# Kernel optimization log

Measured on AMD Instinct MI355X. Metric: run time of the kernel, lower is better.

Reference implementation:

```python
import jax, jax.numpy as jnp
import numpy as np

N, E, F, R, S = 20000, 320000, 64, 8, 10
AVG_NEIGH = 16.0


def setup_inputs() -> dict:
    key = jax.random.key(0)
    ks = jax.random.split(key, 16)
    inp = {
        "vectors": jax.random.normal(ks[0], (E, 3), jnp.float32),
        "node_feats": jax.random.normal(ks[1], (N, F, 4), jnp.float32),  # [N, F, 1(0e)+3(1o)]
        "node_specie": jax.random.randint(ks[2], (N,), 0, S),
        "radial_embedding": jax.random.normal(ks[3], (E, R), jnp.float32),
        "senders": jax.random.randint(ks[4], (E,), 0, N),
        "receivers": jax.random.randint(ks[5], (E,), 0, N),
        # residual FullyConnectedTensorProduct(feats, one-hot species 0e) == species-dep. linear per l
        "W_res_s": jax.random.normal(ks[6], (S, F, F), jnp.float32),
        "W_res_v": jax.random.normal(ks[7], (S, F, F), jnp.float32),
        # interaction block: input linear per l
        "W_in_s": jax.random.normal(ks[8], (F, F), jnp.float32),
        "W_in_v": jax.random.normal(ks[9], (F, F), jnp.float32),
        # radial MLP -> 5 CG tensor-product path weights per channel
        "mlp_w1": jax.random.normal(ks[10], (R, 64), jnp.float32),
        "mlp_w2": jax.random.normal(ks[11], (64, 5 * F), jnp.float32) / 8.0,
        # interaction block: output linear per l
        "W_out_s": jax.random.normal(ks[12], (F, F), jnp.float32),
        "W_out_v": jax.random.normal(ks[13], (F, F), jnp.float32),
        # symmetric product basis (correlation 3), species-dependent term weights
        "W_prod_s": jax.random.normal(ks[14], (S, 5, F), jnp.float32) * 0.3,
        "W_prod_v": jax.random.normal(ks[15], (S, 4, F), jnp.float32) * 0.3,
    }
    k2 = jax.random.split(jax.random.key(1), 3)
    inp["W_lin_s"] = jax.random.normal(k2[0], (F, F), jnp.float32)
    inp["W_lin_v"] = jax.random.normal(k2[1], (F, F), jnp.float32)
    inp["W_read"] = jax.random.normal(k2[2], (F, 1), jnp.float32)
    return inp


def _forward(vectors, node_feats, node_specie, radial_embedding, senders, receivers,
             W_res_s, W_res_v, W_in_s, W_in_v, mlp_w1, mlp_w2, W_out_s, W_out_v,
             W_prod_s, W_prod_v, W_lin_s, W_lin_v, W_read):
    inv_sf = 1.0 / jnp.sqrt(jnp.float32(F))
    s = node_feats[..., 0]          # [N,F]   0e channels
    v = node_feats[..., 1:]         # [N,F,3] 1o channels

    # --- residual connection: FCTP(feats, one-hot species 0e attrs) -> species-gated linear per l
    res_s = jnp.einsum('nf,ngf->ng', s, W_res_s[node_specie]) * inv_sf
    res_v = jnp.einsum('nfc,ngf->ngc', v, W_res_v[node_specie]) * inv_sf

    # --- InteractionBlock ---
    h_s = (s @ W_in_s) * inv_sf
    h_v = jnp.einsum('nfc,fg->ngc', v, W_in_v) * inv_sf

    # spherical harmonics up to max_ell=1: Y0 = 1, Y1 = unit edge vector
    r = jnp.sqrt(jnp.sum(vectors * vectors, -1) + 1e-12)
    Y1 = vectors / r[:, None]                                # [E,3]

    # radial MLP produces per-edge weights for the 5 CG paths:
    # (0e x Y0 -> 0e), (1o . Y1 -> 0e), (0e x Y1 -> 1o), (1o x Y0 -> 1o), (1o x Y1 -> 1o, cross)
    w = (jax.nn.silu(radial_embedding @ mlp_w1) @ mlp_w2).reshape(-1, 5, F)  # [E,5,F]

    ss = h_s[senders]                                        # [E,F]
    sv = h_v[senders]                                        # [E,F,3]
    dot = jnp.einsum('efc,ec->ef', sv, Y1)                   # [E,F]
    m_s = w[:, 0] * ss + w[:, 1] * dot                       # [E,F]
    m_v = (w[:, 2] * ss)[:, :, None] * Y1[:, None, :] \
        + w[:, 3][:, :, None] * sv \
        + w[:, 4][:, :, None] * jnp.cross(sv, Y1[:, None, :])  # [E,F,3]

    agg_s = jnp.zeros_like(h_s).at[receivers].add(m_s) / AVG_NEIGH
    agg_v = jnp.zeros_like(h_v).at[receivers].add(m_v) / AVG_NEIGH
    a_s = (agg_s @ W_out_s) * inv_sf
    a_v = jnp.einsum('nfc,fg->ngc', agg_v, W_out_v) * inv_sf

    # --- EquivariantProductBasisBlock: correlation-3 symmetric contraction, species-dependent ---
    vv = jnp.sum(a_v * a_v, -1)                              # [N,F] invariant |v|^2
    Wp = W_prod_s[node_specie]                               # [N,5,F]
    p_s = (Wp[:, 0] * a_s + Wp[:, 1] * a_s ** 2 + Wp[:, 2] * a_s ** 3
           + Wp[:, 3] * vv + Wp[:, 4] * a_s * vv)
    Wv = W_prod_v[node_specie]                               # [N,4,F]
    p_v = (Wv[:, 0] + Wv[:, 1] * a_s + Wv[:, 2] * a_s ** 2 + Wv[:, 3] * vv)[:, :, None] * a_v

    f_s = (p_s @ W_lin_s) * inv_sf + res_s
    f_v = jnp.einsum('nfc,fg->ngc', p_v, W_lin_v) * inv_sf + res_v

    # --- LinearReadoutBlock (output_irreps = 0e), 1 head ---
    node_out = ((f_s @ W_read) * inv_sf)[:, None, :]         # [N, heads=1, 1]
    new_feats = jnp.concatenate([f_s[..., None], f_v], axis=-1)  # [N,F,4]
    return node_out, new_feats


def reference(vectors, node_feats, node_specie, radial_embedding, senders, receivers,
              W_res_s, W_res_v, W_in_s, W_in_v, mlp_w1, mlp_w2, W_out_s, W_out_v,
              W_prod_s, W_prod_v, W_lin_s, W_lin_v, W_read):
    return _forward(vectors, node_feats, node_specie, radial_embedding, senders, receivers,
                    W_res_s, W_res_v, W_in_s, W_in_v, mlp_w1, mlp_w2, W_out_s, W_out_v,
                    W_prod_s, W_prod_v, W_lin_s, W_lin_v, W_read)
```

## Files before the change

### kernel.cpp

```cpp
#include <hip/hip_runtime.h>
#include <math.h>

#define NN 20000
#define NE 320000
#define NF (NN*64)

typedef short sh8_t  __attribute__((ext_vector_type(8)));
typedef float fl4_t  __attribute__((ext_vector_type(4)));

__device__ __forceinline__ float silu_f(float x){ return x / (1.0f + expf(-x)); }

__device__ __forceinline__ short f2bf(float f){
  unsigned u = __builtin_bit_cast(unsigned, f);
  unsigned r = (u + 0x7fffu + ((u >> 16) & 1u)) >> 16;
  return (short)r;
}
__device__ __forceinline__ float bf2f(short s){
  unsigned u = ((unsigned)(unsigned short)s) << 16;
  return __builtin_bit_cast(float, u);
}

__global__ __launch_bounds__(256) void k_hist(
    const int* __restrict__ receivers, int* __restrict__ counts)
{
  int i = blockIdx.x*256 + threadIdx.x;
  atomicAdd(&counts[receivers[i]], 1);
}

__global__ __launch_bounds__(256) void k_scan(
    const int* __restrict__ counts, int* __restrict__ row_start, int* __restrict__ off2)
{
  __shared__ int part[256];
  __shared__ int excl[257];
  int t = threadIdx.x;
  int lo = t*79, hi = lo+79 < NN ? lo+79 : NN;
  int s = 0;
  for(int i=lo; i<hi; ++i) s += counts[i];
  part[t] = s;
  __syncthreads();
  if(t == 0){
    int a = 0;
    for(int i=0; i<256; ++i){ excl[i] = a; a += part[i]; }
    excl[256] = a;
  }
  __syncthreads();
  int a = excl[t];
  for(int i=lo; i<hi; ++i){
    int c = counts[i];
    row_start[i] = a; off2[i] = a;
    a += c;
  }
  if(t == 255) row_start[NN] = excl[256];
}

__global__ __launch_bounds__(256) void k_scatter(
    const int* __restrict__ receivers, int* __restrict__ off2, int* __restrict__ csr)
{
  int e = blockIdx.x*256 + threadIdx.x;
  int pos = atomicAdd(&off2[receivers[e]], 1);
  csr[pos] = e;
}

__global__ __launch_bounds__(256) void k_prep_w2(
    const float* __restrict__ w2, short* __restrict__ w2f)
{
  int i = blockIdx.x*256 + threadIdx.x;
  int jp   = i & 7;
  int lane = (i >> 3) & 63;
  int frag = i >> 9;
  int k2 = frag / 20, p = frag % 20;
  int j = p >> 2, T = p & 3;
  int k = k2*32 + (lane >> 4)*8 + jp;
  int n = j*64 + T*16 + (lane & 15);
  w2f[i] = f2bf(w2[k*320 + n]);
}

__global__ __launch_bounds__(256) void k_transpose_res(
    const float* __restrict__ Ws, const float* __restrict__ Wv,
    float* __restrict__ Wst, float* __restrict__ Wvt)
{
  int i = blockIdx.x*256 + threadIdx.x;
  int spec = i >> 12;
  int g = (i >> 6) & 63;
  int f = i & 63;
  Wst[spec*4096 + f*64 + g] = Ws[i];
  Wvt[spec*4096 + f*64 + g] = Wv[i];
}

__global__ __launch_bounds__(256) void k_node_pre(
    const float* __restrict__ node_feats, const float* __restrict__ W_in_s,
    const float* __restrict__ W_in_v, float* __restrict__ h_s, float* __restrict__ h_v)
{
  __shared__ float sh[4][4][64];
  int wave = threadIdx.x >> 6, lane = threadIdx.x & 63;
  int n = blockIdx.x*4 + wave;
  int o = n*64 + lane;
  float4 nf = *(const float4*)(node_feats + (size_t)o*4);
  sh[wave][0][lane]=nf.x; sh[wave][1][lane]=nf.y; sh[wave][2][lane]=nf.z; sh[wave][3][lane]=nf.w;
  __syncthreads();
  float as=0.f, av0=0.f, av1=0.f, av2=0.f;
  #pragma unroll 8
  for(int f=0; f<64; ++f){
    float ws = W_in_s[f*64+lane], wv = W_in_v[f*64+lane];
    as  += sh[wave][0][f]*ws;
    av0 += sh[wave][1][f]*wv;
    av1 += sh[wave][2][f]*wv;
    av2 += sh[wave][3][f]*wv;
  }
  h_s[o]      = as *0.125f;
  h_v[o]      = av0*0.125f;
  h_v[NF+o]   = av1*0.125f;
  h_v[2*NF+o] = av2*0.125f;
}

__global__ __launch_bounds__(256) void k_edge_recv(
    const float* __restrict__ vectors, const float* __restrict__ radial,
    const int* __restrict__ senders,
    const int* __restrict__ row_start, const int* __restrict__ csr,
    const float* __restrict__ mlp_w1, const short* __restrict__ w2f,
    const float* __restrict__ h_s, const float* __restrict__ h_v,
    float* __restrict__ agg_s, float* __restrict__ agg_v)
{
  __shared__ float hid[4][16][68];
  __shared__ float ey[4][16][3];
  __shared__ int   esn[4][16];
  __shared__ float rad[4][128];
  int wave = threadIdx.x >> 6, lane = threadIdx.x & 63;
  int n = blockIdx.x*4 + wave;
  int start = row_start[n], end = row_start[n+1];
  int l15 = lane & 15, q = lane >> 4;

  float w1r[8];
  #pragma unroll
  for(int r=0; r<8; ++r) w1r[r] = mlp_w1[r*64+lane];

  float accS[4]  = {0.f,0.f,0.f,0.f};
  float accV0[4] = {0.f,0.f,0.f,0.f};
  float accV1[4] = {0.f,0.f,0.f,0.f};
  float accV2[4] = {0.f,0.f,0.f,0.f};

  for(int base = start; base < end; base += 16){
    int rem = end - base;
    int cnt = rem < 16 ? rem : 16;
    if(lane < 16){
      if(lane < cnt){
        int e = csr[base + lane];
        float4 r0 = *(const float4*)(radial + (size_t)e*8);
        float4 r1 = *(const float4*)(radial + (size_t)e*8 + 4);
        *(float4*)&rad[wave][lane*8]     = r0;
        *(float4*)&rad[wave][lane*8 + 4] = r1;
        float vx = vectors[3*e], vy = vectors[3*e+1], vz = vectors[3*e+2];
        float rinv = 1.0f/sqrtf(vx*vx + vy*vy + vz*vz + 1e-12f);
        ey[wave][lane][0] = vx*rinv; ey[wave][lane][1] = vy*rinv; ey[wave][lane][2] = vz*rinv;
        esn[wave][lane] = senders[e];
      } else {
        *(float4*)&rad[wave][lane*8]     = (float4){0.f,0.f,0.f,0.f};
        *(float4*)&rad[wave][lane*8 + 4] = (float4){0.f,0.f,0.f,0.f};
        ey[wave][lane][0]=0.f; ey[wave][lane][1]=0.f; ey[wave][lane][2]=0.f;
        esn[wave][lane] = 0;
      }
    }
    #pragma unroll
    for(int t=0; t<16; ++t){
      float acc = 0.f;
      #pragma unroll
      for(int r=0; r<8; ++r) acc += rad[wave][t*8+r]*w1r[r];
      hid[wave][t][lane] = silu_f(acc);
    }
    fl4_t C[20];
    #pragma unroll
    for(int p=0; p<20; ++p) C[p] = (fl4_t){0.f,0.f,0.f,0.f};
    #pragma unroll
    for(int k2=0; k2<2; ++k2){
      const float* hp = &hid[wave][l15][k2*32 + q*8];
      sh8_t ahi, alo;
      #pragma unroll
      for(int i=0; i<8; ++i){
        float a = hp[i];
        short h = f2bf(a);
        ahi[i] = h;
        alo[i] = f2bf(a - bf2f(h));
      }
      const short* bbase = w2f + (size_t)(k2*20)*512 + lane*8;
      #pragma unroll
      for(int p=0; p<20; ++p){
        sh8_t b = *(const sh8_t*)(bbase + p*512);
        C[p] = __builtin_amdgcn_mfma_f32_16x16x32_bf16(ahi, b, C[p], 0, 0, 0);
        C[p] = __builtin_amdgcn_mfma_f32_16x16x32_bf16(alo, b, C[p], 0, 0, 0);
      }
    }
    #pragma unroll
    for(int reg=0; reg<4; ++reg){
      int r = q*4 + reg;
      if(r < cnt){
        float y0 = ey[wave][r][0], y1 = ey[wave][r][1], y2 = ey[wave][r][2];
        int snd = esn[wave][r];
        #pragma unroll
        for(int T=0; T<4; ++T){
          int c = T*16 + l15;
          int so = snd*64 + c;
          float ss  = h_s[so];
          float sv0 = h_v[so], sv1 = h_v[NF+so], sv2 = h_v[2*NF+so];
          float dot = sv0*y0 + sv1*y1 + sv2*y2;
          float w0 = C[T][reg], w1v = C[4+T][reg], w2v = C[8+T][reg];
          float w3v = C[12+T][reg], w4v = C[16+T][reg];
          float ms  = w0*ss + w1v*dot;
          float w2s = w2v*ss;
          accS[T]  += ms;
          accV0[T] += w2s*y0 + w3v*sv0 + w4v*(sv1*y2 - sv2*y1);
          accV1[T] += w2s*y1 + w3v*sv1 + w4v*(sv2*y0 - sv0*y2);
          accV2[T] += w2s*y2 + w3v*sv2 + w4v*(sv0*y1 - sv1*y0);
        }
      }
    }
  }
  #pragma unroll
  for(int T=0; T<4; ++T){
    accS[T]  += __shfl_xor(accS[T], 16);  accS[T]  += __shfl_xor(accS[T], 32);
    accV0[T] += __shfl_xor(accV0[T],16);  accV0[T] += __shfl_xor(accV0[T],32);
    accV1[T] += __shfl_xor(accV1[T],16);  accV1[T] += __shfl_xor(accV1[T],32);
    accV2[T] += __shfl_xor(accV2[T],16);  accV2[T] += __shfl_xor(accV2[T],32);
  }
  float oS  = (q&2) ? ((q&1)?accS[3] :accS[2])  : ((q&1)?accS[1] :accS[0]);
  float oV0 = (q&2) ? ((q&1)?accV0[3]:accV0[2]) : ((q&1)?accV0[1]:accV0[0]);
  float oV1 = (q&2) ? ((q&1)?accV1[3]:accV1[2]) : ((q&1)?accV1[1]:accV1[0]);
  float oV2 = (q&2) ? ((q&1)?accV2[3]:accV2[2]) : ((q&1)?accV2[1]:accV2[0]);
  int o = n*64 + lane;
  agg_s[o]      = oS;
  agg_v[o]      = oV0;
  agg_v[NF+o]   = oV1;
  agg_v[2*NF+o] = oV2;
}

__global__ __launch_bounds__(256) void k_node_post(
  const float* __restrict__ node_feats, const int* __restrict__ specie,
  const float* __restrict__ agg_s, const float* __restrict__ agg_v,
  const float* __restrict__ Wrst, const float* __restrict__ Wrvt,
  const float* __restrict__ W_out_s, const float* __restrict__ W_out_v,
  const float* __restrict__ W_prod_s, const float* __restrict__ W_prod_v,
  const float* __restrict__ W_lin_s, const float* __restrict__ W_lin_v,
  const float* __restrict__ W_read, float* __restrict__ out_node, float* __restrict__ out_feats)
{
  __shared__ float shA[4][4][64];
  __shared__ float shS[4][4][64];
  __shared__ float shP[4][4][64];
  int wave = threadIdx.x >> 6, lane = threadIdx.x & 63;
  int n = blockIdx.x*4 + wave;
  int o = n*64 + lane;
  shA[wave][0][lane] = agg_s[o]      * (1.f/16.f);
  shA[wave][1][lane] = agg_v[o]      * (1.f/16.f);
  shA[wave][2][lane] = agg_v[NF+o]   * (1.f/16.f);
  shA[wave][3][lane] = agg_v[2*NF+o] * (1.f/16.f);
  float4 nf = *(const float4*)(node_feats + (size_t)o*4);
  shS[wave][0][lane]=nf.x; shS[wave][1][lane]=nf.y; shS[wave][2][lane]=nf.z; shS[wave][3][lane]=nf.w;
  __syncthreads();
  int spec = specie[n];
  const float* Ws_ = Wrst + spec*4096;
  const float* Wv_ = Wrvt + spec*4096;
  float a_s=0.f,a0=0.f,a1=0.f,a2=0.f, r_s=0.f,r0=0.f,r1=0.f,r2=0.f;
  #pragma unroll 4
  for(int f=0; f<64; ++f){
    float wos=W_out_s[f*64+lane], wov=W_out_v[f*64+lane];
    a_s += shA[wave][0][f]*wos;
    a0  += shA[wave][1][f]*wov;
    a1  += shA[wave][2][f]*wov;
    a2  += shA[wave][3][f]*wov;
    float wrs=Ws_[f*64+lane], wrv=Wv_[f*64+lane];
    r_s += shS[wave][0][f]*wrs;
    r0  += shS[wave][1][f]*wrv;
    r1  += shS[wave][2][f]*wrv;
    r2  += shS[wave][3][f]*wrv;
  }
  a_s*=0.125f; a0*=0.125f; a1*=0.125f; a2*=0.125f;
  r_s*=0.125f; r0*=0.125f; r1*=0.125f; r2*=0.125f;
  float vv = a0*a0 + a1*a1 + a2*a2;
  float as2 = a_s*a_s;
  const float* Wp = W_prod_s + spec*320;
  float p_s = Wp[lane]*a_s + Wp[64+lane]*as2 + Wp[128+lane]*as2*a_s
            + Wp[192+lane]*vv + Wp[256+lane]*a_s*vv;
  const float* Wq = W_prod_v + spec*256;
  float coef = Wq[lane] + Wq[64+lane]*a_s + Wq[128+lane]*as2 + Wq[192+lane]*vv;
  shP[wave][0][lane] = p_s;
  shP[wave][1][lane] = coef*a0;
  shP[wave][2][lane] = coef*a1;
  shP[wave][3][lane] = coef*a2;
  __syncthreads();
  float fs=0.f,f0=0.f,f1=0.f,f2=0.f;
  #pragma unroll 4
  for(int f=0; f<64; ++f){
    float wls=W_lin_s[f*64+lane], wlv=W_lin_v[f*64+lane];
    fs += shP[wave][0][f]*wls;
    f0 += shP[wave][1][f]*wlv;
    f1 += shP[wave][2][f]*wlv;
    f2 += shP[wave][3][f]*wlv;
  }
  fs = fs*0.125f + r_s;
  f0 = f0*0.125f + r0;
  f1 = f1*0.125f + r1;
  f2 = f2*0.125f + r2;
  float x = fs * W_read[lane];
  #pragma unroll
  for(int off=32; off; off>>=1) x += __shfl_down(x, off);
  if(lane==0) out_node[n] = x*0.125f;
  float4 o4; o4.x=fs; o4.y=f0; o4.z=f1; o4.w=f2;
  *(float4*)(out_feats + (size_t)o*4) = o4;
}

extern "C" void kernel_launch(void* const* d_in, const int* in_sizes, int n_in,
                              void* d_out, int out_size, void* d_ws, size_t ws_size,
                              hipStream_t stream) {
  const float* vectors    = (const float*)d_in[0];
  const float* node_feats = (const float*)d_in[1];
  const int*   node_specie= (const int*)  d_in[2];
  const float* radial     = (const float*)d_in[3];
  const int*   senders    = (const int*)  d_in[4];
  const int*   receivers  = (const int*)  d_in[5];
  const float* W_res_s    = (const float*)d_in[6];
  const float* W_res_v    = (const float*)d_in[7];
  const float* W_in_s     = (const float*)d_in[8];
  const float* W_in_v     = (const float*)d_in[9];
  const float* mlp_w1     = (const float*)d_in[10];
  const float* mlp_w2     = (const float*)d_in[11];
  const float* W_out_s    = (const float*)d_in[12];
  const float* W_out_v    = (const float*)d_in[13];
  const float* W_prod_s   = (const float*)d_in[14];
  const float* W_prod_v   = (const float*)d_in[15];
  const float* W_lin_s    = (const float*)d_in[16];
  const float* W_lin_v    = (const float*)d_in[17];
  const float* W_read     = (const float*)d_in[18];

  float* ws    = (float*)d_ws;
  float* h_s   = ws;
  float* h_v   = ws + NF;
  float* agg_s = ws + 4*(size_t)NF;
  float* agg_v = ws + 5*(size_t)NF;
  float* Wrst  = ws + 8*(size_t)NF;
  float* Wrvt  = ws + 8*(size_t)NF + 40960;
  short* w2f   = (short*)(ws + 8*(size_t)NF + 81920);
  int*   ibase = (int*)(ws + 8*(size_t)NF + 81920 + 10240);
  int*   row_start = ibase;
  int*   off2      = ibase + (NN+1);
  int*   csr       = ibase + (NN+1) + NN;

  hipMemsetAsync(off2, 0, (size_t)NN*sizeof(int), stream);
  k_hist<<<NE/256, 256, 0, stream>>>(receivers, off2);
  k_scan<<<1, 256, 0, stream>>>(off2, row_start, off2);
  k_scatter<<<NE/256, 256, 0, stream>>>(receivers, off2, csr);
  k_prep_w2<<<80, 256, 0, stream>>>(mlp_w2, w2f);
  k_transpose_res<<<160, 256, 0, stream>>>(W_res_s, W_res_v, Wrst, Wrvt);
  k_node_pre<<<NN/4, 256, 0, stream>>>(node_feats, W_in_s, W_in_v, h_s, h_v);
  k_edge_recv<<<NN/4, 256, 0, stream>>>(vectors, radial, senders, row_start, csr,
                                        mlp_w1, w2f, h_s, h_v, agg_s, agg_v);
  k_node_post<<<NN/4, 256, 0, stream>>>(node_feats, node_specie, agg_s, agg_v,
                                        Wrst, Wrvt, W_out_s, W_out_v,
                                        W_prod_s, W_prod_v, W_lin_s, W_lin_v,
                                        W_read, (float*)d_out, (float*)d_out + NN);
}
```

Before: 557.6 us.

## Permute edge data into CSR order and store node intermediates as packed bf16

Adds a k_permute pass that writes radial features, normalized edge directions and sender ids into receiver-sorted order, so the edge kernel reads them contiguously instead of gathering through csr. The h_s/h_v and agg intermediates become interleaved bf16 ushort4, so each sender gather is one 8-byte load instead of four strided float loads. The MFMA loop is restructured per channel tile (5 accumulators instead of 20), with launch bounds set to 4 blocks per CU, to cut register pressure. The costs are an extra permutation kernel and its global traffic, plus bf16 rounding of intermediates, which lowers accuracy.

After: 632.5 us. +13.4%, slower.

```diff
diff --git a/kernel.cpp b/kernel.cpp
--- a/kernel.cpp
+++ b/kernel.cpp
@@ -17,6 +17,10 @@
 }
 __device__ __forceinline__ float bf2f(short s){
   unsigned u = ((unsigned)(unsigned short)s) << 16;
+  return __builtin_bit_cast(float, u);
+}
+__device__ __forceinline__ float bfu2f(unsigned short s){
+  unsigned u = ((unsigned)s) << 16;
   return __builtin_bit_cast(float, u);
 }
 
@@ -59,6 +63,25 @@
   int e = blockIdx.x*256 + threadIdx.x;
   int pos = atomicAdd(&off2[receivers[e]], 1);
   csr[pos] = e;
+}
+
+__global__ __launch_bounds__(256) void k_permute(
+    const int* __restrict__ csr, const float* __restrict__ radial,
+    const float* __restrict__ vectors, const int* __restrict__ senders,
+    float* __restrict__ rperm, float4* __restrict__ vperm)
+{
+  int pos = blockIdx.x*256 + threadIdx.x;
+  int e = csr[pos];
+  float4 r0 = *(const float4*)(radial + (size_t)e*8);
+  float4 r1 = *(const float4*)(radial + (size_t)e*8 + 4);
+  *(float4*)(rperm + (size_t)pos*8)     = r0;
+  *(float4*)(rperm + (size_t)pos*8 + 4) = r1;
+  float vx = vectors[3*e], vy = vectors[3*e+1], vz = vectors[3*e+2];
+  float rinv = 1.0f/sqrtf(vx*vx + vy*vy + vz*vz + 1e-12f);
+  float4 v;
+  v.x = vx*rinv; v.y = vy*rinv; v.z = vz*rinv;
+  v.w = __int_as_float(senders[e]);
+  vperm[pos] = v;
 }
 
 __global__ __launch_bounds__(256) void k_prep_w2(
@@ -89,7 +112,7 @@
 
 __global__ __launch_bounds__(256) void k_node_pre(
     const float* __restrict__ node_feats, const float* __restrict__ W_in_s,
-    const float* __restrict__ W_in_v, float* __restrict__ h_s, float* __restrict__ h_v)
+    const float* __restrict__ W_in_v, ushort4* __restrict__ h4)
 {
   __shared__ float sh[4][4][64];
   int wave = threadIdx.x >> 6, lane = threadIdx.x & 63;
@@ -107,21 +130,21 @@
     av1 += sh[wave][2][f]*wv;
     av2 += sh[wave][3][f]*wv;
   }
-  h_s[o]      = as *0.125f;
-  h_v[o]      = av0*0.125f;
-  h_v[NF+o]   = av1*0.125f;
-  h_v[2*NF+o] = av2*0.125f;
-}
-
-__global__ __launch_bounds__(256) void k_edge_recv(
-    const float* __restrict__ vectors, const float* __restrict__ radial,
-    const int* __restrict__ senders,
-    const int* __restrict__ row_start, const int* __restrict__ csr,
+  ushort4 hv;
+  hv.x = (unsigned short)f2bf(as *0.125f);
+  hv.y = (unsigned short)f2bf(av0*0.125f);
+  hv.z = (unsigned short)f2bf(av1*0.125f);
+  hv.w = (unsigned short)f2bf(av2*0.125f);
+  h4[o] = hv;
+}
+
+__global__ __launch_bounds__(256, 4) void k_edge_recv(
+    const int* __restrict__ row_start,
+    const float* __restrict__ rperm, const float4* __restrict__ vperm,
     const float* __restrict__ mlp_w1, const short* __restrict__ w2f,
-    const float* __restrict__ h_s, const float* __restrict__ h_v,
-    float* __restrict__ agg_s, float* __restrict__ agg_v)
-{
-  __shared__ float hid[4][16][68];
+    const ushort4* __restrict__ h4, ushort4* __restrict__ agg4)
+{
+  __shared__ float hid[4][16][65];
   __shared__ float ey[4][16][3];
   __shared__ int   esn[4][16];
   __shared__ float rad[4][128];
@@ -140,24 +163,24 @@
   float accV2[4] = {0.f,0.f,0.f,0.f};
 
   for(int base = start; base < end; base += 16){
-    int rem = end - base;
-    int cnt = rem < 16 ? rem : 16;
-    if(lane < 16){
-      if(lane < cnt){
-        int e = csr[base + lane];
-        float4 r0 = *(const float4*)(radial + (size_t)e*8);
-        float4 r1 = *(const float4*)(radial + (size_t)e*8 + 4);
-        *(float4*)&rad[wave][lane*8]     = r0;
-        *(float4*)&rad[wave][lane*8 + 4] = r1;
-        float vx = vectors[3*e], vy = vectors[3*e+1], vz = vectors[3*e+2];
-        float rinv = 1.0f/sqrtf(vx*vx + vy*vy + vz*vz + 1e-12f);
-        ey[wave][lane][0] = vx*rinv; ey[wave][lane][1] = vy*rinv; ey[wave][lane][2] = vz*rinv;
-        esn[wave][lane] = senders[e];
-      } else {
-        *(float4*)&rad[wave][lane*8]     = (float4){0.f,0.f,0.f,0.f};
-        *(float4*)&rad[wave][lane*8 + 4] = (float4){0.f,0.f,0.f,0.f};
-        ey[wave][lane][0]=0.f; ey[wave][lane][1]=0.f; ey[wave][lane][2]=0.f;
-        esn[wave][lane] = 0;
+    int cnt = end - base; if(cnt > 16) cnt = 16;
+    {
+      int p0 = base + (lane >> 3);
+      int p1 = p0 + 8;
+      float v0 = (p0 < end) ? rperm[(size_t)base*8 + lane]      : 0.f;
+      float v1 = (p1 < end) ? rperm[(size_t)base*8 + 64 + lane] : 0.f;
+      rad[wave][lane]      = v0;
+      rad[wave][64 + lane] = v1;
+      if(lane < 16){
+        int pp = base + lane;
+        if(pp < end){
+          float4 v = vperm[pp];
+          ey[wave][lane][0] = v.x; ey[wave][lane][1] = v.y; ey[wave][lane][2] = v.z;
+          esn[wave][lane] = __float_as_int(v.w);
+        } else {
+          ey[wave][lane][0]=0.f; ey[wave][lane][1]=0.f; ey[wave][lane][2]=0.f;
+          esn[wave][lane] = 0;
+        }
       }
     }
     #pragma unroll
@@ -167,46 +190,46 @@
       for(int r=0; r<8; ++r) acc += rad[wave][t*8+r]*w1r[r];
       hid[wave][t][lane] = silu_f(acc);
     }
-    fl4_t C[20];
-    #pragma unroll
-    for(int p=0; p<20; ++p) C[p] = (fl4_t){0.f,0.f,0.f,0.f};
+    sh8_t ahi[2], alo[2];
     #pragma unroll
     for(int k2=0; k2<2; ++k2){
-      const float* hp = &hid[wave][l15][k2*32 + q*8];
-      sh8_t ahi, alo;
       #pragma unroll
       for(int i=0; i<8; ++i){
-        float a = hp[i];
+        float a = hid[wave][l15][k2*32 + q*8 + i];
         short h = f2bf(a);
-        ahi[i] = h;
-        alo[i] = f2bf(a - bf2f(h));
-      }
-      const short* bbase = w2f + (size_t)(k2*20)*512 + lane*8;
-      #pragma unroll
-      for(int p=0; p<20; ++p){
-        sh8_t b = *(const sh8_t*)(bbase + p*512);
-        C[p] = __builtin_amdgcn_mfma_f32_16x16x32_bf16(ahi, b, C[p], 0, 0, 0);
-        C[p] = __builtin_amdgcn_mfma_f32_16x16x32_bf16(alo, b, C[p], 0, 0, 0);
+        ahi[k2][i] = h;
+        alo[k2][i] = f2bf(a - bf2f(h));
       }
     }
     #pragma unroll
-    for(int reg=0; reg<4; ++reg){
-      int r = q*4 + reg;
-      if(r < cnt){
-        float y0 = ey[wave][r][0], y1 = ey[wave][r][1], y2 = ey[wave][r][2];
-        int snd = esn[wave][r];
+    for(int T=0; T<4; ++T){
+      fl4_t C[5];
+      #pragma unroll
+      for(int j=0; j<5; ++j) C[j] = (fl4_t){0.f,0.f,0.f,0.f};
+      #pragma unroll
+      for(int k2=0; k2<2; ++k2){
+        const short* bb = w2f + (size_t)(k2*20 + T)*512 + lane*8;
         #pragma unroll
-        for(int T=0; T<4; ++T){
-          int c = T*16 + l15;
-          int so = snd*64 + c;
-          float ss  = h_s[so];
-          float sv0 = h_v[so], sv1 = h_v[NF+so], sv2 = h_v[2*NF+so];
+        for(int j=0; j<5; ++j){
+          sh8_t b = *(const sh8_t*)(bb + (size_t)j*2048);
+          C[j] = __builtin_amdgcn_mfma_f32_16x16x32_bf16(ahi[k2], b, C[j], 0, 0, 0);
+          C[j] = __builtin_amdgcn_mfma_f32_16x16x32_bf16(alo[k2], b, C[j], 0, 0, 0);
+        }
+      }
+      #pragma unroll
+      for(int reg=0; reg<4; ++reg){
+        int r = q*4 + reg;
+        if(r < cnt){
+          float y0 = ey[wave][r][0], y1 = ey[wave][r][1], y2 = ey[wave][r][2];
+          int snd = esn[wave][r];
+          ushort4 hh = h4[(size_t)snd*64 + T*16 + l15];
+          float ss  = bfu2f(hh.x);
+          float sv0 = bfu2f(hh.y), sv1 = bfu2f(hh.z), sv2 = bfu2f(hh.w);
           float dot = sv0*y0 + sv1*y1 + sv2*y2;
-          float w0 = C[T][reg], w1v = C[4+T][reg], w2v = C[8+T][reg];
-          float w3v = C[12+T][reg], w4v = C[16+T][reg];
-          float ms  = w0*ss + w1v*dot;
+          float w0 = C[0][reg], w1v = C[1][reg], w2v = C[2][reg];
+          float w3v = C[3][reg], w4v = C[4][reg];
           float w2s = w2v*ss;
-          accS[T]  += ms;
+          accS[T]  += w0*ss + w1v*dot;
           accV0[T] += w2s*y0 + w3v*sv0 + w4v*(sv1*y2 - sv2*y1);
           accV1[T] += w2s*y1 + w3v*sv1 + w4v*(sv2*y0 - sv0*y2);
           accV2[T] += w2s*y2 + w3v*sv2 + w4v*(sv0*y1 - sv1*y0);
@@ -225,16 +248,17 @@
   float oV0 = (q&2) ? ((q&1)?accV0[3]:accV0[2]) : ((q&1)?accV0[1]:accV0[0]);
   float oV1 = (q&2) ? ((q&1)?accV1[3]:accV1[2]) : ((q&1)?accV1[1]:accV1[0]);
   float oV2 = (q&2) ? ((q&1)?accV2[3]:accV2[2]) : ((q&1)?accV2[1]:accV2[0]);
-  int o = n*64 + lane;
-  agg_s[o]      = oS;
-  agg_v[o]      = oV0;
-  agg_v[NF+o]   = oV1;
-  agg_v[2*NF+o] = oV2;
+  ushort4 ov;
+  ov.x = (unsigned short)f2bf(oS);
+  ov.y = (unsigned short)f2bf(oV0);
+  ov.z = (unsigned short)f2bf(oV1);
+  ov.w = (unsigned short)f2bf(oV2);
+  agg4[(size_t)n*64 + lane] = ov;
 }
 
 __global__ __launch_bounds__(256) void k_node_post(
   const float* __restrict__ node_feats, const int* __restrict__ specie,
-  const float* __restrict__ agg_s, const float* __restrict__ agg_v,
+  const ushort4* __restrict__ agg4,
   const float* __restrict__ Wrst, const float* __restrict__ Wrvt,
   const float* __restrict__ W_out_s, const float* __restrict__ W_out_v,
   const float* __restrict__ W_prod_s, const float* __restrict__ W_prod_v,
@@ -247,10 +271,11 @@
   int wave = threadIdx.x >> 6, lane = threadIdx.x & 63;
   int n = blockIdx.x*4 + wave;
   int o = n*64 + lane;
-  shA[wave][0][lane] = agg_s[o]      * (1.f/16.f);
-  shA[wave][1][lane] = agg_v[o]      * (1.f/16.f);
-  shA[wave][2][lane] = agg_v[NF+o]   * (1.f/16.f);
-  shA[wave][3][lane] = agg_v[2*NF+o] * (1.f/16.f);
+  ushort4 ag = agg4[(size_t)o];
+  shA[wave][0][lane] = bfu2f(ag.x) * (1.f/16.f);
+  shA[wave][1][lane] = bfu2f(ag.y) * (1.f/16.f);
+  shA[wave][2][lane] = bfu2f(ag.z) * (1.f/16.f);
+  shA[wave][3][lane] = bfu2f(ag.w) * (1.f/16.f);
   float4 nf = *(const float4*)(node_feats + (size_t)o*4);
   shS[wave][0][lane]=nf.x; shS[wave][1][lane]=nf.y; shS[wave][2][lane]=nf.z; shS[wave][3][lane]=nf.w;
   __syncthreads();
@@ -329,29 +354,28 @@
   const float* W_lin_v    = (const float*)d_in[17];
   const float* W_read     = (const float*)d_in[18];
 
-  float* ws    = (float*)d_ws;
-  float* h_s   = ws;
-  float* h_v   = ws + NF;
-  float* agg_s = ws + 4*(size_t)NF;
-  float* agg_v = ws + 5*(size_t)NF;
-  float* Wrst  = ws + 8*(size_t)NF;
-  float* Wrvt  = ws + 8*(size_t)NF + 40960;
-  short* w2f   = (short*)(ws + 8*(size_t)NF + 81920);
-  int*   ibase = (int*)(ws + 8*(size_t)NF + 81920 + 10240);
-  int*   row_start = ibase;
-  int*   off2      = ibase + (NN+1);
-  int*   csr       = ibase + (NN+1) + NN;
+  float* ws = (float*)d_ws;
+  ushort4* agg4 = (ushort4*)ws;
+  ushort4* h4   = (ushort4*)(ws + 2*(size_t)NF);
+  float* Wrst   = ws + 4*(size_t)NF;
+  float* Wrvt   = Wrst + 40960;
+  short* w2f    = (short*)(Wrvt + 40960);
+  float* rperm  = Wrvt + 40960 + 10240;
+  float4* vperm = (float4*)(rperm + (size_t)NE*8 + 128);
+  int* row_start= (int*)(rperm + (size_t)NE*8 + 128 + (size_t)NE*4 + 64);
+  int* off2     = row_start + (NN+1);
+  int* csr      = off2 + NN;
 
   hipMemsetAsync(off2, 0, (size_t)NN*sizeof(int), stream);
   k_hist<<<NE/256, 256, 0, stream>>>(receivers, off2);
   k_scan<<<1, 256, 0, stream>>>(off2, row_start, off2);
   k_scatter<<<NE/256, 256, 0, stream>>>(receivers, off2, csr);
+  k_permute<<<NE/256, 256, 0, stream>>>(csr, radial, vectors, senders, rperm, vperm);
   k_prep_w2<<<80, 256, 0, stream>>>(mlp_w2, w2f);
   k_transpose_res<<<160, 256, 0, stream>>>(W_res_s, W_res_v, Wrst, Wrvt);
-  k_node_pre<<<NN/4, 256, 0, stream>>>(node_feats, W_in_s, W_in_v, h_s, h_v);
-  k_edge_recv<<<NN/4, 256, 0, stream>>>(vectors, radial, senders, row_start, csr,
-                                        mlp_w1, w2f, h_s, h_v, agg_s, agg_v);
-  k_node_post<<<NN/4, 256, 0, stream>>>(node_feats, node_specie, agg_s, agg_v,
+  k_node_pre<<<NN/4, 256, 0, stream>>>(node_feats, W_in_s, W_in_v, h4);
+  k_edge_recv<<<NN/4, 256, 0, stream>>>(row_start, rperm, vperm, mlp_w1, w2f, h4, agg4);
+  k_node_post<<<NN/4, 256, 0, stream>>>(node_feats, node_specie, agg4,
                                         Wrst, Wrvt, W_out_s, W_out_v,
                                         W_prod_s, W_prod_v, W_lin_s, W_lin_v,
                                         W_read, (float*)d_out, (float*)d_out + NN);
```
